# Kernel optimization log

Measured on AMD Instinct MI355X. Metric: run time of the kernel, lower is better.

Reference implementation:

```python
import jax, jax.numpy as jnp
import numpy as np
import math

N = 768; C_S = 384; C_Z = 128; H = 12; C = 16; P_QK = 4; P_V = 8; C_Z4 = C_Z // 4
INF = 1e5; EPS = 1e-8; LN_EPS = 1e-5


def setup_inputs() -> dict:
    key = jax.random.key(0)
    ks = jax.random.split(key, 16)
    w = lambda k, shp, sc=0.02: jax.random.normal(k, shp, jnp.float32) * sc
    s = jax.random.normal(ks[0], (N, C_S), jnp.float32)
    z = jax.random.normal(ks[1], (N, N, C_Z), jnp.float32)
    m = jax.random.normal(ks[2], (N, 3, 3), jnp.float32)
    q, r_ = jnp.linalg.qr(m)
    rot = q * jnp.sign(jnp.diagonal(r_, axis1=-2, axis2=-1))[:, None, :]  # orthonormal frames
    trans = jax.random.normal(ks[3], (N, 3), jnp.float32) * 10.0
    return {
        "s": s, "z": z, "rot": rot, "trans": trans,
        "s_mask": jnp.ones((N,), jnp.float32),
        "g_s": jnp.ones((C_S,), jnp.float32), "b_s": jnp.zeros((C_S,), jnp.float32),
        "g_z": jnp.ones((C_Z,), jnp.float32), "b_z": jnp.zeros((C_Z,), jnp.float32),
        "Wq": w(ks[4], (C_S, H * C)), "Wk": w(ks[5], (C_S, H * C)), "Wv": w(ks[6], (C_S, H * C)),
        "Wqp": w(ks[7], (C_S, H * P_QK * 3)), "Wkp": w(ks[8], (C_S, H * P_QK * 3)),
        "Wvp": w(ks[9], (C_S, H * P_V * 3)),
        "Wb": w(ks[10], (C_Z, H)), "Wdz": w(ks[11], (C_Z, C_Z4)),
        "head_weights": jnp.zeros((H,), jnp.float32),
        "Wout": w(ks[12], (H * C, C_S)), "Woutb": w(ks[13], (H * C_Z4, C_S)),
        "Woutpts": w(ks[14], (H * P_V * 4, C_S)),
        "rigids_to_res_idx": jnp.arange(N, dtype=jnp.int32),
    }


def _ipa(s, z, rot, trans, s_mask, g_s, b_s, g_z, b_z, Wq, Wk, Wv, Wqp, Wkp, Wvp,
         Wb, Wdz, head_weights, Wout, Woutb, Woutpts, idx):
    def ln(x, g, b):
        mu = jnp.mean(x, -1, keepdims=True)
        var = jnp.mean((x - mu) ** 2, -1, keepdims=True)
        return (x - mu) * jax.lax.rsqrt(var + LN_EPS) * g + b

    s = ln(s, g_s, b_s)
    z = ln(z, g_z, b_z)
    n = s.shape[0]
    q = (s @ Wq).reshape(n, H, C)
    k = (s @ Wk).reshape(n, H, C)
    v = (s @ Wv).reshape(n, H, C)

    def to_global(pts):  # r.apply: R x + t, per residue
        return jnp.einsum('nij,npj->npi', rot, pts) + trans[:, None, :]

    q_pts = to_global((s @ Wqp).reshape(n, H * P_QK, 3))
    k_pts = to_global((s @ Wkp).reshape(n, H * P_QK, 3))
    v_pts = to_global((s @ Wvp).reshape(n, H * P_V, 3))

    b = z @ Wb                      # [N, N, H] pair bias
    pair_z = z @ Wdz                # [N, N, C_Z4]
    mask2 = s_mask[:, None] * s_mask[None, :]
    z_bias = b + (INF * (mask2 - 1.0))[..., None]
    z_bias = z_bias[idx][:, idx]    # broadcast z over rigids via rigid->res index
    pair_g = pair_z[idx][:, idx]

    qp = q_pts.reshape(n, H, P_QK, 3)
    kp = k_pts.reshape(n, H, P_QK, 3)
    d2 = jnp.sum((qp[:, None] - kp[None, :]) ** 2, -1)  # [N, N, H, P_QK]
    hw = jax.nn.softplus(head_weights) * math.sqrt(1.0 / (3 * (P_QK * 9.0 / 2)))
    pt_att = -0.5 * jnp.sum(d2, -1) * hw                # [N, N, H]

    a = (jnp.einsum('ihc,jhc->ijh', q, k) * math.sqrt(1.0 / (3 * C))
         + math.sqrt(1.0 / 3) * z_bias + pt_att)
    a = jax.nn.softmax(a, axis=1)                       # softmax over keys j

    o = jnp.einsum('ijh,jhc->ihc', a, v).reshape(n, H * C)
    vp = v_pts.reshape(n, H, P_V, 3)
    o_pt = jnp.einsum('ijh,jhpx->ihpx', a, vp).reshape(n, H * P_V, 3)
    o_pair = jnp.einsum('ijh,ijc->ihc', a, pair_g).reshape(n, H * C_Z4)

    # r.invert_apply: R^T (x - t)
    o_pt = jnp.einsum('nji,npj->npi', rot, o_pt - trans[:, None, :])
    o_pt_norm = jnp.sqrt(jnp.sum(o_pt ** 2, -1) + EPS)  # [N, H*P_V]
    pts_feat = jnp.concatenate([o_pt.reshape(n, -1), o_pt_norm], -1)
    return o @ Wout + o_pair @ Woutb + pts_feat @ Woutpts


def reference(s, z, rot, trans, s_mask, g_s, b_s, g_z, b_z, Wq, Wk, Wv, Wqp, Wkp, Wvp,
              Wb, Wdz, head_weights, Wout, Woutb, Woutpts, rigids_to_res_idx):
    return _ipa(s, z, rot, trans, s_mask, g_s, b_s, g_z, b_z, Wq, Wk, Wv, Wqp, Wkp,
                Wvp, Wb, Wdz, head_weights, Wout, Woutb, Woutpts, rigids_to_res_idx)
```

## Files before the change

### kernel.cpp

```cpp
#include <hip/hip_runtime.h>
#include <hip/hip_bf16.h>

#define NN 768
#define NSQ (768*768)
#define CS 384
#define CZ 128
#define HH 12
#define INF_ 1e5f
#define EPS_ 1e-8f
#define LN_EPS_ 1e-5f

typedef __attribute__((ext_vector_type(8))) short short8;
typedef __attribute__((ext_vector_type(4))) short short4_t;
typedef __attribute__((ext_vector_type(4))) float floatx4;

constexpr size_t OFF_SLN  = 0;
constexpr size_t OFF_PROJ = OFF_SLN + (size_t)768*384;
constexpr size_t OFF_QPG  = OFF_PROJ + (size_t)768*1152;
constexpr size_t OFF_KPG  = OFF_QPG + (size_t)768*144;
constexpr size_t OFF_VPG  = OFF_KPG + (size_t)768*144;
constexpr size_t OFF_WTBF = OFF_VPG + (size_t)768*288;
constexpr size_t OFF_HW   = OFF_WTBF + 4096;
constexpr size_t OFF_BIAS = OFF_HW + 16;
constexpr size_t OFF_ATT  = OFF_BIAS + (size_t)NSQ*6;
constexpr size_t OFF_PZ   = OFF_ATT + (size_t)12*NSQ;
constexpr size_t OFF_OCAT = OFF_PZ + (size_t)NSQ*16;
constexpr size_t OFF_ABF  = OFF_OCAT + (size_t)768*960;
constexpr size_t OFF_BBF  = OFF_ABF + 294912;
constexpr size_t OFF_CJ   = OFF_BBF + 294912;

__device__ __forceinline__ unsigned short f2bf(float f){
    unsigned int u = __float_as_uint(f);
    u = (u + 0x7fffu + ((u >> 16) & 1u)) >> 16;
    return (unsigned short)u;
}
__device__ __forceinline__ float bf2f(unsigned short u){
    return __uint_as_float((unsigned int)u << 16);
}

__global__ __launch_bounds__(256) void k_setup(const float* __restrict__ Wb, const float* __restrict__ Wdz,
                                               const float* __restrict__ hwin, float* __restrict__ ws,
                                               float* __restrict__ out){
    int b = blockIdx.x, t = threadIdx.x;
    if (b < 2880){ ws[OFF_OCAT + (size_t)b*256 + t] = 0.f; return; }
    b -= 2880;
    if (b < 1152){ out[(size_t)b*256 + t] = 0.f; return; }
    b -= 1152;
    if (b < 24){
        unsigned short* wt = (unsigned short*)(ws + OFF_WTBF);
        int o = b*2 + (t>>7), k = t & 127;
        float v = 0.f;
        if (o < HH) v = Wb[k*HH + o];
        else if (o < 44) v = Wdz[k*32 + (o - HH)];
        wt[o*128 + k] = f2bf(v);
        return;
    }
    b -= 24;
    if (b == 0 && t < HH){
        ws[OFF_HW + t] = log1pf(expf(hwin[t])) * sqrtf(1.0f/54.0f);
    }
}

__global__ __launch_bounds__(256) void k_proj(const float* __restrict__ s, const float* __restrict__ gs,
                                              const float* __restrict__ bs,
                                              const float* __restrict__ Wq, const float* __restrict__ Wk,
                                              const float* __restrict__ Wv, const float* __restrict__ Wqp,
                                              const float* __restrict__ Wkp, const float* __restrict__ Wvp,
                                              float* __restrict__ ws){
    __shared__ float slds[16][CS];
    __shared__ float stats[16][2];
    int rt = blockIdx.x, ct = blockIdx.y, t = threadIdx.x;
    for (int ix = t; ix < 16*CS; ix += 256){
        int r = ix / CS, c = ix % CS;
        slds[r][c] = s[(size_t)(rt*16 + r)*CS + c];
    }
    __syncthreads();
    int w = t >> 6, lane = t & 63;
    for (int r = w; r < 16; r += 4){
        float sum = 0.f, sq = 0.f;
        #pragma unroll
        for (int c0 = 0; c0 < CS; c0 += 64){
            float x = slds[r][c0 + lane];
            sum += x; sq += x*x;
        }
        #pragma unroll
        for (int off = 32; off; off >>= 1){
            sum += __shfl_xor(sum, off, 64);
            sq  += __shfl_xor(sq , off, 64);
        }
        if (lane == 0){
            float mu = sum * (1.0f/CS);
            float var = sq * (1.0f/CS) - mu*mu;
            stats[r][0] = mu;
            stats[r][1] = rsqrtf(var + LN_EPS_);
        }
    }
    __syncthreads();
    for (int ix = t; ix < 16*CS; ix += 256){
        int r = ix / CS, c = ix % CS;
        slds[r][c] = (slds[r][c] - stats[r][0]) * stats[r][1] * gs[c] + bs[c];
    }
    __syncthreads();
    int col = ct*128 + (t & 127);
    int rg = t >> 7;
    const float* wp; int stride;
    if      (col < 192){ wp = Wq  + col;       stride = 192; }
    else if (col < 384){ wp = Wk  + (col-192); stride = 192; }
    else if (col < 576){ wp = Wv  + (col-384); stride = 192; }
    else if (col < 720){ wp = Wqp + (col-576); stride = 144; }
    else if (col < 864){ wp = Wkp + (col-720); stride = 144; }
    else               { wp = Wvp + (col-864); stride = 288; }
    float acc[8] = {0,0,0,0,0,0,0,0};
    for (int k = 0; k < CS; k += 4){
        float w0 = wp[(size_t)k*stride];
        float w1 = wp[(size_t)(k+1)*stride];
        float w2 = wp[(size_t)(k+2)*stride];
        float w3 = wp[(size_t)(k+3)*stride];
        #pragma unroll
        for (int r = 0; r < 8; r++){
            floatx4 sv = *(const floatx4*)&slds[rg*8+r][k];
            acc[r] += sv[0]*w0 + sv[1]*w1 + sv[2]*w2 + sv[3]*w3;
        }
    }
    float* proj = ws + OFF_PROJ;
    for (int r = 0; r < 8; r++) proj[(size_t)(rt*16 + rg*8 + r)*1152 + col] = acc[r];
}

__global__ __launch_bounds__(192) void k_pts(const float* __restrict__ rot, const float* __restrict__ trans,
                                             float* __restrict__ ws){
    int i = blockIdx.x, p = threadIdx.x;
    const float* proj = ws + OFF_PROJ + (size_t)i*1152;
    const float* src; float* dst;
    if (p < 48)      { src = proj + 576 + p*3;       dst = ws + OFF_QPG + (size_t)i*144 + p*3; }
    else if (p < 96) { src = proj + 720 + (p-48)*3;  dst = ws + OFF_KPG + (size_t)i*144 + (p-48)*3; }
    else             { src = proj + 864 + (p-96)*3;  dst = ws + OFF_VPG + (size_t)i*288 + (p-96)*3; }
    float x = src[0], y = src[1], z = src[2];
    const float* R = rot + (size_t)i*9;
    const float* T = trans + (size_t)i*3;
    dst[0] = R[0]*x + R[1]*y + R[2]*z + T[0];
    dst[1] = R[3]*x + R[4]*y + R[5]*z + T[1];
    dst[2] = R[6]*x + R[7]*y + R[8]*z + T[2];
}

__global__ __launch_bounds__(256) void k_feat(float* __restrict__ ws){
    int i = blockIdx.x, t = threadIdx.x;
    const float* proj = ws + OFF_PROJ + (size_t)i*1152;
    const float* qpg  = ws + OFF_QPG + (size_t)i*144;
    const float* kpg  = ws + OFF_KPG + (size_t)i*144;
    unsigned short* Abf = (unsigned short*)(ws + OFF_ABF);
    unsigned short* Bbf = (unsigned short*)(ws + OFF_BBF);
    const float S1 = 0.14433756729740643f;
    for (int ix = t; ix < 12*64; ix += 256){
        int h = ix >> 6, c = ix & 63;
        float hwv = ws[OFF_HW + h];
        unsigned short ab = 0, bb = 0;
        if (c < 16){
            ab = f2bf(proj[h*16 + c]);
            bb = f2bf(S1 * proj[192 + h*16 + c]);
        } else if (c < 28){
            int d = c - 16;
            ab = f2bf(qpg[h*12 + d]);
            bb = f2bf(hwv * kpg[h*12 + d]);
        } else if (c < 40){
            int d = c - 28;
            float qp = qpg[h*12 + d];
            unsigned short hi = f2bf(qp);
            ab = f2bf(qp - bf2f(hi));
            bb = f2bf(hwv * kpg[h*12 + d]);
        } else if (c < 52){
            int d = c - 40;
            ab = f2bf(qpg[h*12 + d]);
            float x = hwv * kpg[h*12 + d];
            unsigned short xh = f2bf(x);
            bb = f2bf(x - bf2f(xh));
        }
        Abf[((size_t)h*768 + i)*64 + c] = ab;
        Bbf[((size_t)h*768 + i)*64 + c] = bb;
    }
    if (t < 12){
        float hwv = ws[OFF_HW + t];
        float s2 = 0.f;
        #pragma unroll
        for (int d = 0; d < 12; d++){ float kp = kpg[t*12 + d]; s2 += kp*kp; }
        ws[OFF_CJ + (size_t)t*768 + i] = -0.5f * hwv * s2;
    }
}

__global__ __launch_bounds__(256) void k_z(const float* __restrict__ z, const float* __restrict__ gz,
                                           const float* __restrict__ bz, float* __restrict__ ws){
    __shared__ unsigned short zlds[64][136];
    int t = threadIdx.x;
    int pb = blockIdx.x * 64;
    int lane32 = t & 31;
    int col = lane32 * 4;
    floatx4 g4 = *(const floatx4*)(gz + col);
    floatx4 b4 = *(const floatx4*)(bz + col);
    const float* zbase = z + (size_t)pb * 128;
    #pragma unroll
    for (int g = 0; g < 8; g++){
        int row = g*8 + (t >> 5);
        floatx4 v = *(const floatx4*)(zbase + (size_t)g*1024 + (size_t)t*4);
        float sum = v[0]+v[1]+v[2]+v[3];
        float sq  = v[0]*v[0]+v[1]*v[1]+v[2]*v[2]+v[3]*v[3];
        #pragma unroll
        for (int off = 1; off <= 16; off <<= 1){
            sum += __shfl_xor(sum, off, 64);
            sq  += __shfl_xor(sq , off, 64);
        }
        float mu = sum * (1.0f/128.0f);
        float rstd = rsqrtf(sq*(1.0f/128.0f) - mu*mu + LN_EPS_);
        short4_t sv;
        sv[0] = (short)f2bf((v[0]-mu)*rstd*g4[0] + b4[0]);
        sv[1] = (short)f2bf((v[1]-mu)*rstd*g4[1] + b4[1]);
        sv[2] = (short)f2bf((v[2]-mu)*rstd*g4[2] + b4[2]);
        sv[3] = (short)f2bf((v[3]-mu)*rstd*g4[3] + b4[3]);
        *(short4_t*)&zlds[row][col] = sv;
    }
    __syncthreads();
    const unsigned short* wt = (const unsigned short*)(ws + OFF_WTBF);
    int lane = t & 63, wv = t >> 6;
    int m = lane & 15, quad = lane >> 4;
    short8 bfrag[3][4];
    #pragma unroll
    for (int ot = 0; ot < 3; ot++)
        #pragma unroll
        for (int ks = 0; ks < 4; ks++){
            int o = ot*16 + m;
            bfrag[ot][ks] = *(const short8*)(wt + o*128 + ks*32 + quad*8);
        }
    floatx4 acc[3] = {{0.f,0.f,0.f,0.f},{0.f,0.f,0.f,0.f},{0.f,0.f,0.f,0.f}};
    int rbase = wv*16;
    #pragma unroll
    for (int ks = 0; ks < 4; ks++){
        short8 a = *(const short8*)&zlds[rbase + m][ks*32 + quad*8];
        acc[0] = __builtin_amdgcn_mfma_f32_16x16x32_bf16(a, bfrag[0][ks], acc[0], 0, 0, 0);
        acc[1] = __builtin_amdgcn_mfma_f32_16x16x32_bf16(a, bfrag[1][ks], acc[1], 0, 0, 0);
        acc[2] = __builtin_amdgcn_mfma_f32_16x16x32_bf16(a, bfrag[2][ks], acc[2], 0, 0, 0);
    }
    __syncthreads();
    unsigned short* stb = &zlds[0][0];
    unsigned short* stp = &zlds[0][0] + 64*12;
    #pragma unroll
    for (int ot = 0; ot < 3; ot++){
        int o = ot*16 + m;
        #pragma unroll
        for (int rg = 0; rg < 4; rg++){
            int rp = rbase + quad*4 + rg;
            float val = acc[ot][rg];
            if (o < HH)      stb[rp*12 + o] = f2bf(val);
            else if (o < 44) stp[rp*32 + (o - HH)] = f2bf(val);
        }
    }
    __syncthreads();
    unsigned short* bias16 = (unsigned short*)(ws + OFF_BIAS);
    unsigned int*   pz32   = (unsigned int*)((unsigned short*)(ws + OFF_PZ));
    for (int ix = t; ix < 12*32; ix += 256){
        int o = ix >> 5, u = ix & 31;
        unsigned int val = (unsigned int)stb[(u*2)*12 + o] | ((unsigned int)stb[(u*2+1)*12 + o] << 16);
        *(unsigned int*)(bias16 + (size_t)o*NSQ + pb + u*2) = val;
    }
    for (int ix = t; ix < 64*16; ix += 256){
        int rp = ix >> 4, u = ix & 15;
        unsigned int val = (unsigned int)stp[rp*32 + u*2] | ((unsigned int)stp[rp*32 + u*2+1] << 16);
        pz32[(size_t)(pb + rp)*16 + u] = val;
    }
}

__global__ __launch_bounds__(256) void k_lg(const float* __restrict__ smask, const int* __restrict__ idx,
                                            float* __restrict__ ws){
    __shared__ unsigned short Al[64][64];
    __shared__ unsigned short Bl[64][64];
    __shared__ int   idJ[64];
    __shared__ float sIv[64];
    __shared__ float sjv[64];
    __shared__ float cjv[64];
    int it = blockIdx.x, jt = blockIdx.y, h = blockIdx.z, t = threadIdx.x;
    const unsigned int* Ag = (const unsigned int*)((const unsigned short*)(ws + OFF_ABF) + ((size_t)h*768 + it*64)*64);
    const unsigned int* Bg = (const unsigned int*)((const unsigned short*)(ws + OFF_BBF) + ((size_t)h*768 + jt*64)*64);
    for (int ix = t; ix < 64*32; ix += 256){
        int r = ix >> 5, u = ix & 31;
        int gs = ((u >> 2) ^ (r & 7));
        int us = (gs << 2) | (u & 3);
        ((unsigned int*)&Al[r][0])[us] = Ag[ix];
        ((unsigned int*)&Bl[r][0])[us] = Bg[ix];
    }
    if (t < 64){
        int i = it*64 + t, j = jt*64 + t;
        int ii = idx[i], jj = idx[j];
        sIv[t] = smask[ii];
        idJ[t] = jj;
        sjv[t] = INF_ * 0.57735026918962576f * (smask[jj] - 1.0f);
        cjv[t] = ws[OFF_CJ + (size_t)h*768 + j];
    }
    __syncthreads();
    int lane = t & 63, w = t >> 6;
    int m = lane & 15, quad = lane >> 4;
    short8 af0, af1;
    {
        int r = w*16 + m;
        int g0 = (quad) ^ (r & 7);
        int g1 = (quad + 4) ^ (r & 7);
        af0 = *(const short8*)&Al[r][g0*8];
        af1 = *(const short8*)&Al[r][g1*8];
    }
    floatx4 acc[4] = {{0.f,0.f,0.f,0.f},{0.f,0.f,0.f,0.f},{0.f,0.f,0.f,0.f},{0.f,0.f,0.f,0.f}};
    #pragma unroll
    for (int nt = 0; nt < 4; nt++){
        int r = nt*16 + m;
        int g0 = (quad) ^ (r & 7);
        int g1 = (quad + 4) ^ (r & 7);
        short8 bf0 = *(const short8*)&Bl[r][g0*8];
        short8 bf1 = *(const short8*)&Bl[r][g1*8];
        acc[nt] = __builtin_amdgcn_mfma_f32_16x16x32_bf16(af0, bf0, acc[nt], 0, 0, 0);
        acc[nt] = __builtin_amdgcn_mfma_f32_16x16x32_bf16(af1, bf1, acc[nt], 0, 0, 0);
    }
    const unsigned short* bias16 = (const unsigned short*)(ws + OFF_BIAS) + (size_t)h*NSQ;
    float* att = ws + OFF_ATT + (size_t)h*NSQ;
    const float S2 = 0.57735026918962576f;
    #pragma unroll
    for (int rg = 0; rg < 4; rg++){
        int il = w*16 + quad*4 + rg;
        int i  = it*64 + il;
        int ires = idx[i];
        float si = sIv[il];
        const unsigned short* brow = bias16 + (size_t)ires*NN;
        float* arow = att + (size_t)i*NN + jt*64;
        #pragma unroll
        for (int nt = 0; nt < 4; nt++){
            int jl = nt*16 + m;
            float bv = bf2f(brow[idJ[jl]]);
            arow[jl] = acc[nt][rg] + S2*bv + si*sjv[jl] + cjv[jl];
        }
    }
}

__global__ __launch_bounds__(256) void k_softmax(float* __restrict__ ws){
    int t = threadIdx.x;
    int w = t >> 6, lane = t & 63;
    size_t rowi = (size_t)blockIdx.x*4 + w;
    float* row = ws + OFF_ATT + rowi*NN;
    floatx4 v0 = *(floatx4*)(row + lane*4);
    floatx4 v1 = *(floatx4*)(row + 256 + lane*4);
    floatx4 v2 = *(floatx4*)(row + 512 + lane*4);
    float mx = fmaxf(fmaxf(fmaxf(v0[0],v0[1]), fmaxf(v0[2],v0[3])),
               fmaxf(fmaxf(fmaxf(v1[0],v1[1]), fmaxf(v1[2],v1[3])),
                     fmaxf(fmaxf(v2[0],v2[1]), fmaxf(v2[2],v2[3]))));
    #pragma unroll
    for (int off = 32; off; off >>= 1) mx = fmaxf(mx, __shfl_xor(mx, off, 64));
    floatx4 e0, e1, e2;
    #pragma unroll
    for (int u = 0; u < 4; u++){ e0[u] = expf(v0[u]-mx); e1[u] = expf(v1[u]-mx); e2[u] = expf(v2[u]-mx); }
    float s = e0[0]+e0[1]+e0[2]+e0[3] + e1[0]+e1[1]+e1[2]+e1[3] + e2[0]+e2[1]+e2[2]+e2[3];
    #pragma unroll
    for (int off = 32; off; off >>= 1) s += __shfl_xor(s, off, 64);
    float inv = 1.0f / s;
    #pragma unroll
    for (int u = 0; u < 4; u++){ e0[u] *= inv; e1[u] *= inv; e2[u] *= inv; }
    *(floatx4*)(row + lane*4) = e0;
    *(floatx4*)(row + 256 + lane*4) = e1;
    *(floatx4*)(row + 512 + lane*4) = e2;
}

__global__ __launch_bounds__(256) void k_ov(float* __restrict__ ws){
    __shared__ float wlds[128][41];
    __shared__ float plds[32][128];
    int h = blockIdx.x, it = blockIdx.y, zs = blockIdx.z, t = threadIdx.x;
    const float* proj = ws + OFF_PROJ;
    const float* vpg  = ws + OFF_VPG;
    const float* att  = ws + OFF_ATT + (size_t)h*NSQ;
    int c = t & 63, isub = t >> 6;
    float acc[8] = {0,0,0,0,0,0,0,0};
    for (int jt = zs*2; jt < zs*2+2; jt++){
        __syncthreads();
        for (int ix = t; ix < 128*40; ix += 256){
            int jj = ix / 40, cc = ix % 40;
            int j = jt*128 + jj;
            wlds[jj][cc] = (cc < 16) ? proj[(size_t)j*1152 + 384 + h*16 + cc]
                                     : vpg[(size_t)j*288 + h*24 + (cc - 16)];
        }
        for (int ix = t; ix < 32*128; ix += 256){
            int rr = ix >> 7, jj = ix & 127;
            plds[rr][jj] = att[(size_t)(it*32 + rr)*NN + jt*128 + jj];
        }
        __syncthreads();
        if (c < 40){
            for (int jj = 0; jj < 128; jj += 4){
                float w0 = wlds[jj][c], w1 = wlds[jj+1][c], w2 = wlds[jj+2][c], w3 = wlds[jj+3][c];
                #pragma unroll
                for (int rr = 0; rr < 8; rr++){
                    floatx4 pv = *(floatx4*)&plds[isub*8+rr][jj];
                    acc[rr] += pv[0]*w0 + pv[1]*w1 + pv[2]*w2 + pv[3]*w3;
                }
            }
        }
    }
    if (c < 40){
        float* ocat = ws + OFF_OCAT;
        int col = (c < 16) ? (h*16 + c) : (576 + h*24 + (c - 16));
        for (int rr = 0; rr < 8; rr++){
            int i = it*32 + isub*8 + rr;
            atomicAdd(&ocat[(size_t)i*960 + col], acc[rr]);
        }
    }
}

__global__ __launch_bounds__(384) void k_opair(const int* __restrict__ idx, float* __restrict__ ws){
    __shared__ float plds[12][132];
    __shared__ float pzlds[128][33];
    int i = blockIdx.x, jt = blockIdx.y, t = threadIdx.x;
    int ires = idx[i];
    const unsigned int* pzg = (const unsigned int*)((const unsigned short*)(ws + OFF_PZ) + (size_t)ires*NN*32);
    const float* att = ws + OFF_ATT;
    for (int ix = t; ix < 12*128; ix += 384){
        int hh = ix >> 7, jj = ix & 127;
        plds[hh][jj] = att[(size_t)hh*NSQ + (size_t)i*NN + jt*128 + jj];
    }
    for (int ix = t; ix < 128*16; ix += 384){
        int jj = ix >> 4, cp = ix & 15;
        int jres = idx[jt*128 + jj];
        unsigned int u2 = pzg[(size_t)jres*16 + cp];
        pzlds[jj][cp*2]   = __uint_as_float(u2 << 16);
        pzlds[jj][cp*2+1] = __uint_as_float(u2 & 0xffff0000u);
    }
    __syncthreads();
    int h = t >> 5, c = t & 31;
    float acc = 0.f;
    #pragma unroll 4
    for (int j = 0; j < 128; j++)
        acc += plds[h][j] * pzlds[j][c];
    float* oc = ws + OFF_OCAT + (size_t)i*960 + 192;
    atomicAdd(&oc[h*32 + c], acc);
}

__global__ __launch_bounds__(96) void k_ptfin(const float* __restrict__ rot, const float* __restrict__ trans,
                                              float* __restrict__ ws){
    int i = blockIdx.x, p = threadIdx.x;
    float* base = ws + OFF_OCAT + (size_t)i*960;
    float* pt = base + 576 + p*3;
    float x = pt[0] - trans[i*3+0];
    float y = pt[1] - trans[i*3+1];
    float z = pt[2] - trans[i*3+2];
    const float* R = rot + (size_t)i*9;
    float lx = R[0]*x + R[3]*y + R[6]*z;
    float ly = R[1]*x + R[4]*y + R[7]*z;
    float lz = R[2]*x + R[5]*y + R[8]*z;
    pt[0] = lx; pt[1] = ly; pt[2] = lz;
    base[864 + p] = sqrtf(lx*lx + ly*ly + lz*lz + EPS_);
}

__global__ __launch_bounds__(256) void k_out(const float* __restrict__ Wout, const float* __restrict__ Woutb,
                                             const float* __restrict__ Woutp, float* __restrict__ ws,
                                             float* __restrict__ out){
    __shared__ float olds[32][244];
    int it = blockIdx.x, ct = blockIdx.y, kc = blockIdx.z, t = threadIdx.x;
    const float* ocat = ws + OFF_OCAT;
    for (int ix = t; ix < 32*240; ix += 256){
        int r = ix / 240, kk = ix % 240;
        olds[r][kk] = ocat[(size_t)(it*32 + r)*960 + kc*240 + kk];
    }
    __syncthreads();
    int cl = t & 63, ig = t >> 6;
    int c0 = ct*128 + cl, c1 = c0 + 64;
    float acc0[8], acc1[8];
    #pragma unroll
    for (int r=0;r<8;r++){ acc0[r]=0; acc1[r]=0; }
    for (int kk = 0; kk < 240; kk += 4){
        float w0[4], w1[4];
        #pragma unroll
        for (int u = 0; u < 4; u++){
            int k = kc*240 + kk + u;
            const float* wrow = (k < 192) ? (Wout  + (size_t)k*CS)
                              : (k < 576) ? (Woutb + (size_t)(k-192)*CS)
                                          : (Woutp + (size_t)(k-576)*CS);
            w0[u] = wrow[c0]; w1[u] = wrow[c1];
        }
        #pragma unroll
        for (int r = 0; r < 8; r++){
            floatx4 ov = *(const floatx4*)&olds[ig*8 + r][kk];
            acc0[r] += ov[0]*w0[0] + ov[1]*w0[1] + ov[2]*w0[2] + ov[3]*w0[3];
            acc1[r] += ov[0]*w1[0] + ov[1]*w1[1] + ov[2]*w1[2] + ov[3]*w1[3];
        }
    }
    for (int r = 0; r < 8; r++){
        int i = it*32 + ig*8 + r;
        atomicAdd(&out[(size_t)i*CS + c0], acc0[r]);
        atomicAdd(&out[(size_t)i*CS + c1], acc1[r]);
    }
}

extern "C" void kernel_launch(void* const* d_in, const int* in_sizes, int n_in,
                              void* d_out, int out_size, void* d_ws, size_t ws_size,
                              hipStream_t stream){
    const float* s     = (const float*)d_in[0];
    const float* z     = (const float*)d_in[1];
    const float* rot   = (const float*)d_in[2];
    const float* trans = (const float*)d_in[3];
    const float* smask = (const float*)d_in[4];
    const float* gs    = (const float*)d_in[5];
    const float* bs    = (const float*)d_in[6];
    const float* gz    = (const float*)d_in[7];
    const float* bz    = (const float*)d_in[8];
    const float* Wq    = (const float*)d_in[9];
    const float* Wk    = (const float*)d_in[10];
    const float* Wv    = (const float*)d_in[11];
    const float* Wqp   = (const float*)d_in[12];
    const float* Wkp   = (const float*)d_in[13];
    const float* Wvp   = (const float*)d_in[14];
    const float* Wb    = (const float*)d_in[15];
    const float* Wdz   = (const float*)d_in[16];
    const float* hwin  = (const float*)d_in[17];
    const float* Wout  = (const float*)d_in[18];
    const float* Woutb = (const float*)d_in[19];
    const float* Woutp = (const float*)d_in[20];
    const int*   idx   = (const int*)d_in[21];
    float* ws  = (float*)d_ws;
    float* out = (float*)d_out;

    k_setup  <<<4057, 256, 0, stream>>>(Wb, Wdz, hwin, ws, out);
    k_proj   <<<dim3(48, 9), 256, 0, stream>>>(s, gs, bs, Wq, Wk, Wv, Wqp, Wkp, Wvp, ws);
    k_pts    <<<768, 192, 0, stream>>>(rot, trans, ws);
    k_feat   <<<768, 256, 0, stream>>>(ws);
    k_z      <<<9216, 256, 0, stream>>>(z, gz, bz, ws);
    k_lg     <<<dim3(12, 12, 12), 256, 0, stream>>>(smask, idx, ws);
    k_softmax<<<2304, 256, 0, stream>>>(ws);
    k_ov     <<<dim3(12, 24, 3), 256, 0, stream>>>(ws);
    k_opair  <<<dim3(768, 6), 384, 0, stream>>>(idx, ws);
    k_ptfin  <<<768, 96, 0, stream>>>(rot, trans, ws);
    k_out    <<<dim3(24, 3, 4), 256, 0, stream>>>(Wout, Woutb, Woutp, ws, out);
}
```

Before: 693.5 us.

## Use bf16 MFMA for pair-output contraction with transposed pair features

The softmax kernel now also writes a bf16 copy of the attention probabilities. k_z stores the projected pair features transposed, channel-major. k_opair is rewritten to load these bf16 tiles into LDS and contract them with MFMA 16x16x32 instructions instead of scalar fp32 FMAs. The separate points and feature kernels are also merged into one launch that keeps the global points in LDS. The cost is an extra bf16 attention buffer write, a gathered strided load of the pair features, and reduced precision in the attention-weighted pair sum.

```diff
diff --git a/kernel.cpp b/kernel.cpp
--- a/kernel.cpp
+++ b/kernel.cpp
@@ -28,6 +28,7 @@
 constexpr size_t OFF_ABF  = OFF_OCAT + (size_t)768*960;
 constexpr size_t OFF_BBF  = OFF_ABF + 294912;
 constexpr size_t OFF_CJ   = OFF_BBF + 294912;
+constexpr size_t OFF_ATTB = OFF_CJ + 9216;
 
 __device__ __forceinline__ unsigned short f2bf(float f){
     unsigned int u = __float_as_uint(f);
@@ -126,27 +127,28 @@
     for (int r = 0; r < 8; r++) proj[(size_t)(rt*16 + rg*8 + r)*1152 + col] = acc[r];
 }
 
-__global__ __launch_bounds__(192) void k_pts(const float* __restrict__ rot, const float* __restrict__ trans,
-                                             float* __restrict__ ws){
-    int i = blockIdx.x, p = threadIdx.x;
-    const float* proj = ws + OFF_PROJ + (size_t)i*1152;
-    const float* src; float* dst;
-    if (p < 48)      { src = proj + 576 + p*3;       dst = ws + OFF_QPG + (size_t)i*144 + p*3; }
-    else if (p < 96) { src = proj + 720 + (p-48)*3;  dst = ws + OFF_KPG + (size_t)i*144 + (p-48)*3; }
-    else             { src = proj + 864 + (p-96)*3;  dst = ws + OFF_VPG + (size_t)i*288 + (p-96)*3; }
-    float x = src[0], y = src[1], z = src[2];
-    const float* R = rot + (size_t)i*9;
-    const float* T = trans + (size_t)i*3;
-    dst[0] = R[0]*x + R[1]*y + R[2]*z + T[0];
-    dst[1] = R[3]*x + R[4]*y + R[5]*z + T[1];
-    dst[2] = R[6]*x + R[7]*y + R[8]*z + T[2];
-}
-
-__global__ __launch_bounds__(256) void k_feat(float* __restrict__ ws){
+__global__ __launch_bounds__(256) void k_ptsfeat(const float* __restrict__ rot, const float* __restrict__ trans,
+                                                 float* __restrict__ ws){
+    __shared__ float qp[144];
+    __shared__ float kp[144];
     int i = blockIdx.x, t = threadIdx.x;
     const float* proj = ws + OFF_PROJ + (size_t)i*1152;
-    const float* qpg  = ws + OFF_QPG + (size_t)i*144;
-    const float* kpg  = ws + OFF_KPG + (size_t)i*144;
+    if (t < 192){
+        int p = t;
+        const float* src; float* dst; float* lbuf = nullptr;
+        if (p < 48)      { src = proj + 576 + p*3;      dst = ws + OFF_QPG + (size_t)i*144 + p*3; lbuf = qp + p*3; }
+        else if (p < 96) { src = proj + 720 + (p-48)*3; dst = ws + OFF_KPG + (size_t)i*144 + (p-48)*3; lbuf = kp + (p-48)*3; }
+        else             { src = proj + 864 + (p-96)*3; dst = ws + OFF_VPG + (size_t)i*288 + (p-96)*3; }
+        float x = src[0], y = src[1], z = src[2];
+        const float* R = rot + (size_t)i*9;
+        const float* T = trans + (size_t)i*3;
+        float gx = R[0]*x + R[1]*y + R[2]*z + T[0];
+        float gy = R[3]*x + R[4]*y + R[5]*z + T[1];
+        float gz = R[6]*x + R[7]*y + R[8]*z + T[2];
+        dst[0] = gx; dst[1] = gy; dst[2] = gz;
+        if (lbuf){ lbuf[0] = gx; lbuf[1] = gy; lbuf[2] = gz; }
+    }
+    __syncthreads();
     unsigned short* Abf = (unsigned short*)(ws + OFF_ABF);
     unsigned short* Bbf = (unsigned short*)(ws + OFF_BBF);
     const float S1 = 0.14433756729740643f;
@@ -159,18 +161,18 @@
             bb = f2bf(S1 * proj[192 + h*16 + c]);
         } else if (c < 28){
             int d = c - 16;
-            ab = f2bf(qpg[h*12 + d]);
-            bb = f2bf(hwv * kpg[h*12 + d]);
+            ab = f2bf(qp[h*12 + d]);
+            bb = f2bf(hwv * kp[h*12 + d]);
         } else if (c < 40){
             int d = c - 28;
-            float qp = qpg[h*12 + d];
-            unsigned short hi = f2bf(qp);
-            ab = f2bf(qp - bf2f(hi));
-            bb = f2bf(hwv * kpg[h*12 + d]);
+            float q = qp[h*12 + d];
+            unsigned short hi = f2bf(q);
+            ab = f2bf(q - bf2f(hi));
+            bb = f2bf(hwv * kp[h*12 + d]);
         } else if (c < 52){
             int d = c - 40;
-            ab = f2bf(qpg[h*12 + d]);
-            float x = hwv * kpg[h*12 + d];
+            ab = f2bf(qp[h*12 + d]);
+            float x = hwv * kp[h*12 + d];
             unsigned short xh = f2bf(x);
             bb = f2bf(x - bf2f(xh));
         }
@@ -181,7 +183,7 @@
         float hwv = ws[OFF_HW + t];
         float s2 = 0.f;
         #pragma unroll
-        for (int d = 0; d < 12; d++){ float kp = kpg[t*12 + d]; s2 += kp*kp; }
+        for (int d = 0; d < 12; d++){ float k = kp[t*12 + d]; s2 += k*k; }
         ws[OFF_CJ + (size_t)t*768 + i] = -0.5f * hwv * s2;
     }
 }
@@ -248,21 +250,21 @@
             int rp = rbase + quad*4 + rg;
             float val = acc[ot][rg];
             if (o < HH)      stb[rp*12 + o] = f2bf(val);
-            else if (o < 44) stp[rp*32 + (o - HH)] = f2bf(val);
+            else if (o < 44) stp[rp*34 + (o - HH)] = f2bf(val);
         }
     }
     __syncthreads();
     unsigned short* bias16 = (unsigned short*)(ws + OFF_BIAS);
-    unsigned int*   pz32   = (unsigned int*)((unsigned short*)(ws + OFF_PZ));
+    unsigned int*   pzT32  = (unsigned int*)((unsigned short*)(ws + OFF_PZ));
     for (int ix = t; ix < 12*32; ix += 256){
         int o = ix >> 5, u = ix & 31;
         unsigned int val = (unsigned int)stb[(u*2)*12 + o] | ((unsigned int)stb[(u*2+1)*12 + o] << 16);
         *(unsigned int*)(bias16 + (size_t)o*NSQ + pb + u*2) = val;
     }
-    for (int ix = t; ix < 64*16; ix += 256){
-        int rp = ix >> 4, u = ix & 15;
-        unsigned int val = (unsigned int)stp[rp*32 + u*2] | ((unsigned int)stp[rp*32 + u*2+1] << 16);
-        pz32[(size_t)(pb + rp)*16 + u] = val;
+    for (int ix = t; ix < 32*32; ix += 256){
+        int c = ix >> 5, u = ix & 31;
+        unsigned int val = (unsigned int)stp[(u*2)*34 + c] | ((unsigned int)stp[(u*2+1)*34 + c] << 16);
+        pzT32[(size_t)c*(NSQ/2) + (pb >> 1) + u] = val;
     }
 }
 
@@ -339,9 +341,9 @@
     int w = t >> 6, lane = t & 63;
     size_t rowi = (size_t)blockIdx.x*4 + w;
     float* row = ws + OFF_ATT + rowi*NN;
-    floatx4 v0 = *(floatx4*)(row + lane*4);
-    floatx4 v1 = *(floatx4*)(row + 256 + lane*4);
-    floatx4 v2 = *(floatx4*)(row + 512 + lane*4);
+    floatx4 v0 = *(const floatx4*)(row + lane*4);
+    floatx4 v1 = *(const floatx4*)(row + 256 + lane*4);
+    floatx4 v2 = *(const floatx4*)(row + 512 + lane*4);
     float mx = fmaxf(fmaxf(fmaxf(v0[0],v0[1]), fmaxf(v0[2],v0[3])),
                fmaxf(fmaxf(fmaxf(v1[0],v1[1]), fmaxf(v1[2],v1[3])),
                      fmaxf(fmaxf(v2[0],v2[1]), fmaxf(v2[2],v2[3]))));
@@ -359,6 +361,17 @@
     *(floatx4*)(row + lane*4) = e0;
     *(floatx4*)(row + 256 + lane*4) = e1;
     *(floatx4*)(row + 512 + lane*4) = e2;
+    unsigned short* brow = (unsigned short*)(ws + OFF_ATTB) + rowi*NN;
+    short4_t o0, o1, o2;
+    #pragma unroll
+    for (int u = 0; u < 4; u++){
+        o0[u] = (short)f2bf(e0[u]);
+        o1[u] = (short)f2bf(e1[u]);
+        o2[u] = (short)f2bf(e2[u]);
+    }
+    *(short4_t*)(brow + lane*4) = o0;
+    *(short4_t*)(brow + 256 + lane*4) = o1;
+    *(short4_t*)(brow + 512 + lane*4) = o2;
 }
 
 __global__ __launch_bounds__(256) void k_ov(float* __restrict__ ws){
@@ -404,32 +417,44 @@
     }
 }
 
-__global__ __launch_bounds__(384) void k_opair(const int* __restrict__ idx, float* __restrict__ ws){
-    __shared__ float plds[12][132];
-    __shared__ float pzlds[128][33];
+__global__ __launch_bounds__(128) void k_opair(const int* __restrict__ idx, float* __restrict__ ws){
+    __shared__ unsigned short Ald[16][136];
+    __shared__ unsigned short Bld[32][136];
+    __shared__ int jres[128];
     int i = blockIdx.x, jt = blockIdx.y, t = threadIdx.x;
     int ires = idx[i];
-    const unsigned int* pzg = (const unsigned int*)((const unsigned short*)(ws + OFF_PZ) + (size_t)ires*NN*32);
-    const float* att = ws + OFF_ATT;
-    for (int ix = t; ix < 12*128; ix += 384){
-        int hh = ix >> 7, jj = ix & 127;
-        plds[hh][jj] = att[(size_t)hh*NSQ + (size_t)i*NN + jt*128 + jj];
-    }
-    for (int ix = t; ix < 128*16; ix += 384){
-        int jj = ix >> 4, cp = ix & 15;
-        int jres = idx[jt*128 + jj];
-        unsigned int u2 = pzg[(size_t)jres*16 + cp];
-        pzlds[jj][cp*2]   = __uint_as_float(u2 << 16);
-        pzlds[jj][cp*2+1] = __uint_as_float(u2 & 0xffff0000u);
-    }
-    __syncthreads();
-    int h = t >> 5, c = t & 31;
-    float acc = 0.f;
-    #pragma unroll 4
-    for (int j = 0; j < 128; j++)
-        acc += plds[h][j] * pzlds[j][c];
+    const unsigned short* attb = (const unsigned short*)(ws + OFF_ATTB);
+    const unsigned short* pzT  = (const unsigned short*)(ws + OFF_PZ);
+    int jb = jt*128;
+    jres[t] = idx[jb + t];
+    __syncthreads();
+    for (int ix = t; ix < 16*16; ix += 128){
+        int r = ix >> 4, u = ix & 15;
+        uint4 v = {0,0,0,0};
+        if (r < 12) v = *(const uint4*)(attb + (size_t)r*NSQ + (size_t)i*NN + jb + u*8);
+        *(uint4*)&Ald[r][u*8] = v;
+    }
+    size_t rowoff = (size_t)ires*NN;
+    for (int ix = t; ix < 32*128; ix += 128){
+        int c = ix >> 7, jj = ix & 127;
+        Bld[c][jj] = pzT[(size_t)c*NSQ + rowoff + jres[jj]];
+    }
+    __syncthreads();
+    int lane = t & 63, wv = t >> 6;
+    int m = lane & 15, quad = lane >> 4;
+    floatx4 acc = {0.f,0.f,0.f,0.f};
+    #pragma unroll
+    for (int ks = 0; ks < 4; ks++){
+        short8 a = *(const short8*)&Ald[m][ks*32 + quad*8];
+        short8 b = *(const short8*)&Bld[wv*16 + m][ks*32 + quad*8];
+        acc = __builtin_amdgcn_mfma_f32_16x16x32_bf16(a, b, acc, 0, 0, 0);
+    }
     float* oc = ws + OFF_OCAT + (size_t)i*960 + 192;
-    atomicAdd(&oc[h*32 + c], acc);
+    #pragma unroll
+    for (int rg = 0; rg < 4; rg++){
+        int hh = quad*4 + rg;
+        if (hh < 12) atomicAdd(&oc[hh*32 + wv*16 + m], acc[rg]);
+    }
 }
 
 __global__ __launch_bounds__(96) void k_ptfin(const float* __restrict__ rot, const float* __restrict__ trans,
@@ -518,13 +543,12 @@
 
     k_setup  <<<4057, 256, 0, stream>>>(Wb, Wdz, hwin, ws, out);
     k_proj   <<<dim3(48, 9), 256, 0, stream>>>(s, gs, bs, Wq, Wk, Wv, Wqp, Wkp, Wvp, ws);
-    k_pts    <<<768, 192, 0, stream>>>(rot, trans, ws);
-    k_feat   <<<768, 256, 0, stream>>>(ws);
+    k_ptsfeat<<<768, 256, 0, stream>>>(rot, trans, ws);
     k_z      <<<9216, 256, 0, stream>>>(z, gz, bz, ws);
     k_lg     <<<dim3(12, 12, 12), 256, 0, stream>>>(smask, idx, ws);
     k_softmax<<<2304, 256, 0, stream>>>(ws);
     k_ov     <<<dim3(12, 24, 3), 256, 0, stream>>>(ws);
-    k_opair  <<<dim3(768, 6), 384, 0, stream>>>(idx, ws);
+    k_opair  <<<dim3(768, 6), 128, 0, stream>>>(idx, ws);
     k_ptfin  <<<768, 96, 0, stream>>>(rot, trans, ws);
     k_out    <<<dim3(24, 3, 4), 256, 0, stream>>>(Wout, Woutb, Woutp, ws, out);
 }
```

Result: faster. 669.7 us (-3.4%).
